# Kernel optimization log

Hardware: AMD Instinct MI355X
Metric: run time of the kernel (lower is better)

Reference implementation:

```python
import jax, jax.numpy as jnp
import numpy as np

B, S, D, H = 4, 2048, 768, 12
DH = D // H  # 64


def setup_inputs() -> dict:
    key = jax.random.key(0)
    ks = jax.random.split(key, 7)
    return {
        "sequences": jax.random.normal(ks[0], (B, S, D), dtype=jnp.float32),
        "wq": jax.random.normal(ks[1], (H, DH, DH), dtype=jnp.float32) / np.sqrt(DH),
        "bq": jax.random.normal(ks[2], (H, DH), dtype=jnp.float32) * 0.02,
        "wk": jax.random.normal(ks[3], (H, DH, DH), dtype=jnp.float32) / np.sqrt(DH),
        "bk": jax.random.normal(ks[4], (H, DH), dtype=jnp.float32) * 0.02,
        "wv": jax.random.normal(ks[5], (H, DH, DH), dtype=jnp.float32) / np.sqrt(DH),
        "bv": jax.random.normal(ks[6], (H, DH), dtype=jnp.float32) * 0.02,
    }


def reference(sequences, wq, bq, wk, bk, wv, bv):
    # split channels into heads: [B, S, H, DH]
    xh = sequences.reshape(B, S, H, DH)
    # per-head linear projections (weight applied as x @ W^T + b, matching nn.Linear)
    q = jnp.einsum("bshd,hed->bshe", xh, wq) + bq  # [B,S,H,DH]
    k = jnp.einsum("bshd,hed->bshe", xh, wk) + bk
    v = jnp.einsum("bshd,hed->bshe", xh, wv) + bv
    scale = 1.0 / np.sqrt(DH).astype(np.float32)
    scores = jnp.einsum("bqhd,bkhd->bhqk", q, k) * scale  # [B,H,S,S]
    attn = jax.nn.softmax(scores, axis=-1)
    out = jnp.einsum("bhqk,bkhd->bqhd", attn, v)  # [B,S,H,DH]
    return out.reshape(B, S, D)
```

## Files before the change

kernel.cpp:

```cpp
#include <hip/hip_runtime.h>

#define NB 4
#define NS 2048
#define ND 768
#define NH 12
#define NDH 64
#define NT (NS / 128)
#define XPITCH 72
#define SSCALE 0.18033688011112043f

typedef __bf16 bf16x8 __attribute__((ext_vector_type(8)));
typedef float  f32x4  __attribute__((ext_vector_type(4)));
typedef unsigned int u32;

#define MFMA16(a, b, c) __builtin_amdgcn_mfma_f32_16x16x32_bf16(a, b, c, 0, 0, 0)

__device__ __forceinline__ u32 packbf(float a, float b) {
    u32 ua = __builtin_bit_cast(u32, a) + 0x8000u;
    u32 ub = __builtin_bit_cast(u32, b) + 0x8000u;
    return __builtin_amdgcn_perm(ub, ua, 0x07060302u);
}

__device__ __forceinline__ bf16x8 cvt8(float4 a, float4 b) {
    union { u32 u[4]; bf16x8 v; } r;
    r.u[0] = packbf(a.x, a.y); r.u[1] = packbf(a.z, a.w);
    r.u[2] = packbf(b.x, b.y); r.u[3] = packbf(b.z, b.w);
    return r.v;
}

__device__ __forceinline__ __bf16 f2bf(float f) {
    u32 u = __builtin_bit_cast(u32, f) + 0x8000u;
    unsigned short s = (unsigned short)(u >> 16);
    return __builtin_bit_cast(__bf16, s);
}

__global__ __launch_bounds__(256, 4) void proj_kernel(
    const float* __restrict__ x,
    const float* __restrict__ wq, const float* __restrict__ bq,
    const float* __restrict__ wk, const float* __restrict__ bk,
    const float* __restrict__ wv, const float* __restrict__ bv,
    __bf16* __restrict__ qws, __bf16* __restrict__ kws, __bf16* __restrict__ vtws)
{
    const int st = blockIdx.x, h = blockIdx.y, b = blockIdx.z;
    const int s0 = st * 64;
    const int tid = threadIdx.x;

    __shared__ __align__(16) __bf16 Xs[64 * XPITCH];
    __shared__ __align__(16) __bf16 Tv[64 * XPITCH];

    const int r = tid >> 2, f = tid & 3;
    const int lane = tid & 63, w = tid >> 6, col = lane & 15, quad = lane >> 4;

    const size_t wrow = (size_t)(h * NDH + w * 16 + col) * NDH;
    const float* wq0 = wq + wrow + quad * 8;
    const float* wk0 = wk + wrow + quad * 8;
    const float* wv0 = wv + wrow + quad * 8;
    const bf16x8 wqa0 = cvt8(*(const float4*)(wq0),      *(const float4*)(wq0 + 4));
    const bf16x8 wqa1 = cvt8(*(const float4*)(wq0 + 32), *(const float4*)(wq0 + 36));
    const bf16x8 wka0 = cvt8(*(const float4*)(wk0),      *(const float4*)(wk0 + 4));
    const bf16x8 wka1 = cvt8(*(const float4*)(wk0 + 32), *(const float4*)(wk0 + 36));
    const bf16x8 wva0 = cvt8(*(const float4*)(wv0),      *(const float4*)(wv0 + 4));
    const bf16x8 wva1 = cvt8(*(const float4*)(wv0 + 32), *(const float4*)(wv0 + 36));

    float bqs[4], bks[4], bvs[4];
#pragma unroll
    for (int rr = 0; rr < 4; ++rr) {
        const int e = h * NDH + w * 16 + quad * 4 + rr;
        bqs[rr] = bq[e] * SSCALE;
        bks[rr] = bk[e];
        bvs[rr] = bv[e];
    }

    const size_t bh = (size_t)(b * NH + h);

    {
        const float* xrow = x + (size_t)(b * NS + s0 + r) * ND + h * NDH + f * 16;
        const float4 v0 = *(const float4*)(xrow);
        const float4 v1 = *(const float4*)(xrow + 4);
        const float4 v2 = *(const float4*)(xrow + 8);
        const float4 v3 = *(const float4*)(xrow + 12);
        *(bf16x8*)&Xs[r * XPITCH + f * 16]     = cvt8(v0, v1);
        *(bf16x8*)&Xs[r * XPITCH + f * 16 + 8] = cvt8(v2, v3);
    }
    __syncthreads();

#pragma unroll
    for (int nt = 0; nt < 4; ++nt) {
        const bf16x8 xb0 = *(const bf16x8*)&Xs[(nt * 16 + col) * XPITCH + quad * 8];
        const bf16x8 xb1 = *(const bf16x8*)&Xs[(nt * 16 + col) * XPITCH + 32 + quad * 8];
        f32x4 aq = {0.f, 0.f, 0.f, 0.f};
        f32x4 ak = {0.f, 0.f, 0.f, 0.f};
        f32x4 av = {0.f, 0.f, 0.f, 0.f};
        aq = MFMA16(wqa0, xb0, aq); aq = MFMA16(wqa1, xb1, aq);
        ak = MFMA16(wka0, xb0, ak); ak = MFMA16(wka1, xb1, ak);
        av = MFMA16(wva0, xb0, av); av = MFMA16(wva1, xb1, av);

        union { u32 u[2]; uint2 v; } pq, pk;
        pq.u[0] = packbf(fmaf(aq[0], SSCALE, bqs[0]), fmaf(aq[1], SSCALE, bqs[1]));
        pq.u[1] = packbf(fmaf(aq[2], SSCALE, bqs[2]), fmaf(aq[3], SSCALE, bqs[3]));
        pk.u[0] = packbf(ak[0] + bks[0], ak[1] + bks[1]);
        pk.u[1] = packbf(ak[2] + bks[2], ak[3] + bks[3]);
        const size_t goff = (bh * NS + s0 + nt * 16 + col) * NDH + w * 16 + quad * 4;
        *(uint2*)(qws + goff) = pq.v;
        *(uint2*)(kws + goff) = pk.v;

        const int pos = ((nt >> 1) << 5) + ((col >> 2) << 3) + ((nt & 1) << 2) + (col & 3);
#pragma unroll
        for (int rr = 0; rr < 4; ++rr)
            Tv[(w * 16 + quad * 4 + rr) * XPITCH + pos] = f2bf(av[rr] + bvs[rr]);
    }
    __syncthreads();

    {
        const uint4 v0 = *(const uint4*)&Tv[r * XPITCH + f * 16];
        const uint4 v1 = *(const uint4*)&Tv[r * XPITCH + f * 16 + 8];
        __bf16* vdst = vtws + (bh * NDH + r) * NS + s0 + f * 16;
        *(uint4*)vdst = v0; *(uint4*)(vdst + 8) = v1;
    }
}

__global__ __launch_bounds__(256, 3) void attn_kernel(
    const __bf16* __restrict__ qws, const __bf16* __restrict__ kws,
    const __bf16* __restrict__ vtws, float* __restrict__ out)
{
    const int bid = blockIdx.x;
    const int xcd = bid & 7;
    const int j   = bid >> 3;
    const int g   = xcd * 6 + (j >> 5);
    const int qt  = j & 31;
    const int h   = g % NH;
    const int b   = g / NH;

    const int q0 = qt * 64;
    const int tid = threadIdx.x;

    __shared__ __align__(16) unsigned char smem[36864];
    __bf16* lds = (__bf16*)smem;
    float* slabA = (float*)smem;
    float* slabB = (float*)(smem + 17408);
    float* lbuf  = (float*)(smem + 34816);

    const size_t bh = (size_t)(b * NH + h);
    const int lane = tid & 63, w = tid >> 6, col = lane & 15, quad = lane >> 4;
    const int L = lane;

    bf16x8 qb0[4], qb1[4];
#pragma unroll
    for (int nt = 0; nt < 4; ++nt) {
        const __bf16* qp = qws + (bh * NS + q0 + nt * 16 + col) * NDH + quad * 8;
        qb0[nt] = *(const bf16x8*)(qp);
        qb1[nt] = *(const bf16x8*)(qp + 32);
    }

    const __bf16* ksrc = kws + bh * (size_t)(NS * NDH)
                       + (size_t)(w * 32 + (L >> 3)) * NDH + ((L & 7) ^ (L >> 3)) * 8;
    const __bf16* vsrc = vtws + bh * (size_t)(NDH * NS)
                       + (size_t)(L >> 2) * NS + w * 32 + ((L & 3) ^ ((L >> 3) & 3)) * 8;
    const int kb_lds = w * 2048 + L * 8;
    const int vb_lds = 8192 + w * 2048 + L * 8;

    const int cx7 = col & 7;
    int ka_off[2][2], va_off[4];
#pragma unroll
    for (int mt = 0; mt < 2; ++mt) {
        const int base = w * 2048 + (mt * 16 + col) * 64;
        ka_off[mt][0] = base + ((quad)     ^ cx7) * 8;
        ka_off[mt][1] = base + ((quad + 4) ^ cx7) * 8;
    }
#pragma unroll
    for (int dt = 0; dt < 4; ++dt)
        va_off[dt] = 8192 + w * 2048 + (dt * 16 + col) * 32 + (quad ^ ((col >> 1) & 3)) * 8;

    float l[4] = {0.f, 0.f, 0.f, 0.f};
    f32x4 o[4][4];
#pragma unroll
    for (int dt = 0; dt < 4; ++dt)
#pragma unroll
        for (int nt = 0; nt < 4; ++nt) o[dt][nt] = (f32x4){0.f, 0.f, 0.f, 0.f};

    uint4 kstg[4], vstg[4];
#pragma unroll
    for (int i = 0; i < 4; ++i) kstg[i] = *(const uint4*)(ksrc + i * 512);
#pragma unroll
    for (int i = 0; i < 4; ++i) vstg[i] = *(const uint4*)(vsrc + (size_t)i * 16 * NS);
#pragma unroll
    for (int i = 0; i < 4; ++i) *(uint4*)&lds[kb_lds + i * 512] = kstg[i];
#pragma unroll
    for (int i = 0; i < 4; ++i) *(uint4*)&lds[vb_lds + i * 512] = vstg[i];

    for (int kt = 0; kt < NT; ++kt) {
        if (kt + 1 < NT) {
            const __bf16* ks = ksrc + (size_t)(kt + 1) * 8192;
            const __bf16* vs = vsrc + (kt + 1) * 128;
#pragma unroll
            for (int i = 0; i < 4; ++i) kstg[i] = *(const uint4*)(ks + i * 512);
#pragma unroll
            for (int i = 0; i < 4; ++i) vstg[i] = *(const uint4*)(vs + (size_t)i * 16 * NS);
        }

        bf16x8 ka[2][2], va[4];
#pragma unroll
        for (int mt = 0; mt < 2; ++mt) {
            ka[mt][0] = *(const bf16x8*)&lds[ka_off[mt][0]];
            ka[mt][1] = *(const bf16x8*)&lds[ka_off[mt][1]];
        }
#pragma unroll
        for (int dt = 0; dt < 4; ++dt) va[dt] = *(const bf16x8*)&lds[va_off[dt]];

        __builtin_amdgcn_s_setprio(1);
#pragma unroll
        for (int nt = 0; nt < 4; ++nt) {
            f32x4 sA = {0.f, 0.f, 0.f, 0.f};
            f32x4 sB = {0.f, 0.f, 0.f, 0.f};
            sA = MFMA16(ka[0][0], qb0[nt], sA); sA = MFMA16(ka[0][1], qb1[nt], sA);
            sB = MFMA16(ka[1][0], qb0[nt], sB); sB = MFMA16(ka[1][1], qb1[nt], sB);

            const float p0 = __builtin_amdgcn_exp2f(sA[0]);
            const float p1 = __builtin_amdgcn_exp2f(sA[1]);
            const float p2 = __builtin_amdgcn_exp2f(sA[2]);
            const float p3 = __builtin_amdgcn_exp2f(sA[3]);
            const float p4 = __builtin_amdgcn_exp2f(sB[0]);
            const float p5 = __builtin_amdgcn_exp2f(sB[1]);
            const float p6 = __builtin_amdgcn_exp2f(sB[2]);
            const float p7 = __builtin_amdgcn_exp2f(sB[3]);
            l[nt] += ((p0 + p1) + (p2 + p3)) + ((p4 + p5) + (p6 + p7));

            union { u32 u[4]; bf16x8 v; } pb;
            pb.u[0] = packbf(p0, p1);
            pb.u[1] = packbf(p2, p3);
            pb.u[2] = packbf(p4, p5);
            pb.u[3] = packbf(p6, p7);

#pragma unroll
            for (int dt = 0; dt < 4; ++dt)
                o[dt][nt] = MFMA16(va[dt], pb.v, o[dt][nt]);
        }
        __builtin_amdgcn_s_setprio(0);

        if (kt + 1 < NT) {
#pragma unroll
            for (int i = 0; i < 4; ++i) *(uint4*)&lds[kb_lds + i * 512] = kstg[i];
#pragma unroll
            for (int i = 0; i < 4; ++i) *(uint4*)&lds[vb_lds + i * 512] = vstg[i];
        }
    }

#pragma unroll
    for (int nt = 0; nt < 4; ++nt) {
        l[nt] += __shfl_xor(l[nt], 16, 64);
        l[nt] += __shfl_xor(l[nt], 32, 64);
    }

    __syncthreads();
    if (quad == 0) {
#pragma unroll
        for (int nt = 0; nt < 4; ++nt)
            lbuf[w * 64 + nt * 16 + col] = l[nt];
    }
    __syncthreads();

    float scale[4];
#pragma unroll
    for (int nt = 0; nt < 4; ++nt) {
        const int qi = nt * 16 + col;
        const float Lt = (lbuf[qi] + lbuf[64 + qi]) + (lbuf[128 + qi] + lbuf[192 + qi]);
        scale[nt] = 1.0f / Lt;
    }
    __syncthreads();
#pragma unroll
    for (int dt = 0; dt < 4; ++dt)
#pragma unroll
        for (int nt = 0; nt < 4; ++nt) o[dt][nt] *= scale[nt];

    if (w == 0 || w == 2) {
        float* s = (w == 0) ? slabA : slabB;
#pragma unroll
        for (int dt = 0; dt < 4; ++dt)
#pragma unroll
            for (int nt = 0; nt < 4; ++nt)
                *(f32x4*)&s[(nt * 16 + col) * 68 + dt * 16 + quad * 4] = o[dt][nt];
    }
    __syncthreads();
    if (w == 1 || w == 3) {
        float* s = (w == 1) ? slabA : slabB;
#pragma unroll
        for (int dt = 0; dt < 4; ++dt)
#pragma unroll
            for (int nt = 0; nt < 4; ++nt) {
                f32x4* p = (f32x4*)&s[(nt * 16 + col) * 68 + dt * 16 + quad * 4];
                *p = *p + o[dt][nt];
            }
    }
    __syncthreads();

    const int qr = tid >> 2, fq = tid & 3;
#pragma unroll
    for (int j2 = 0; j2 < 4; ++j2) {
        const f32x4 a = *(const f32x4*)&slabA[qr * 68 + fq * 16 + j2 * 4];
        const f32x4 c = *(const f32x4*)&slabB[qr * 68 + fq * 16 + j2 * 4];
        *(f32x4*)&out[(size_t)(b * NS + q0 + qr) * ND + h * NDH + fq * 16 + j2 * 4] = a + c;
    }
}

extern "C" void kernel_launch(void* const* d_in, const int* in_sizes, int n_in,
                              void* d_out, int out_size, void* d_ws, size_t ws_size,
                              hipStream_t stream) {
    (void)in_sizes; (void)n_in; (void)out_size; (void)ws_size;
    const float* x  = (const float*)d_in[0];
    const float* wq = (const float*)d_in[1];
    const float* bq = (const float*)d_in[2];
    const float* wk = (const float*)d_in[3];
    const float* bk = (const float*)d_in[4];
    const float* wv = (const float*)d_in[5];
    const float* bv = (const float*)d_in[6];
    float* out = (float*)d_out;

    __bf16* qws  = (__bf16*)d_ws;
    __bf16* kws  = qws + (size_t)NB * NH * NS * NDH;
    __bf16* vtws = kws + (size_t)NB * NH * NS * NDH;

    dim3 grid(NS / 64, NH, NB);
    proj_kernel<<<grid, 256, 0, stream>>>(x, wq, bq, wk, bk, wv, bv, qws, kws, vtws);
    attn_kernel<<<dim3(NS / 64 * NH * NB), 256, 0, stream>>>(qws, kws, vtws, out);
}
```

Baseline: 180.8 us.

## Write Q/K/V in MFMA-fragment order and load attention operands directly from global

The projection kernel now writes Q, K and transposed V into a pre-swizzled layout that matches each lane's MFMA operand fragment. The attention kernel drops the LDS staging of K/V and its register-staged copies. It instead loads fragments straight from global memory with coalesced 16-byte reads, double-buffered in registers across two key tiles. This removes LDS writes, reads and bank-conflict swizzling, and the setprio hints are dropped. The trade-off is more direct global/L2 traffic per wave and added register pressure.

```diff
diff --git a/kernel.cpp b/kernel.cpp
--- a/kernel.cpp
+++ b/kernel.cpp
@@ -33,6 +33,7 @@
     unsigned short s = (unsigned short)(u >> 16);
     return __builtin_bit_cast(__bf16, s);
 }
+
 
 __global__ __launch_bounds__(256, 4) void proj_kernel(
     const float* __restrict__ x,
@@ -84,6 +85,13 @@
     }
     __syncthreads();
 
+    const int e0 = w * 16 + quad * 4;
+    const int jj = e0 >> 5;
+    const int qa = (e0 >> 3) & 3;
+    const int hf = (e0 >> 2) & 1;
+    const int Lf = qa * 16 + col;
+    const int kt = st >> 1;
+
 #pragma unroll
     for (int nt = 0; nt < 4; ++nt) {
         const bf16x8 xb0 = *(const bf16x8*)&Xs[(nt * 16 + col) * XPITCH + quad * 8];
@@ -100,9 +108,13 @@
         pq.u[1] = packbf(fmaf(aq[2], SSCALE, bqs[2]), fmaf(aq[3], SSCALE, bqs[3]));
         pk.u[0] = packbf(ak[0] + bks[0], ak[1] + bks[1]);
         pk.u[1] = packbf(ak[2] + bks[2], ak[3] + bks[3]);
-        const size_t goff = (bh * NS + s0 + nt * 16 + col) * NDH + w * 16 + quad * 4;
-        *(uint2*)(qws + goff) = pq.v;
-        *(uint2*)(kws + goff) = pk.v;
+
+        const int wa = (st & 1) * 2 + (nt >> 1);
+        const int mt = nt & 1;
+        const size_t kidx = ((((((size_t)bh * 16 + kt) * 4 + wa) * 2 + mt) * 2 + jj) * 64 + Lf) * 8 + hf * 4;
+        const size_t qidx = (((((size_t)bh * 32 + st) * 4 + nt) * 2 + jj) * 64 + Lf) * 8 + hf * 4;
+        *(uint2*)(kws + kidx) = pk.v;
+        *(uint2*)(qws + qidx) = pq.v;
 
         const int pos = ((nt >> 1) << 5) + ((col >> 2) << 3) + ((nt & 1) << 2) + (col & 3);
 #pragma unroll
@@ -114,8 +126,14 @@
     {
         const uint4 v0 = *(const uint4*)&Tv[r * XPITCH + f * 16];
         const uint4 v1 = *(const uint4*)&Tv[r * XPITCH + f * 16 + 8];
-        __bf16* vdst = vtws + (bh * NDH + r) * NS + s0 + f * 16;
-        *(uint4*)vdst = v0; *(uint4*)(vdst + 8) = v1;
+        const int wv_ = (st & 1) * 2 + (f >> 1);
+        const int dtv = r >> 4;
+        const int colv = r & 15;
+        const int L0 = ((f & 1) * 2 + 0) * 16 + colv;
+        const int L1 = ((f & 1) * 2 + 1) * 16 + colv;
+        const size_t vbase = (((size_t)bh * 16 + kt) * 4 + wv_) * 4 + dtv;
+        *(uint4*)(vtws + (vbase * 64 + L0) * 8) = v0;
+        *(uint4*)(vtws + (vbase * 64 + L1) * 8) = v1;
     }
 }
 
@@ -134,42 +152,26 @@
     const int q0 = qt * 64;
     const int tid = threadIdx.x;
 
-    __shared__ __align__(16) unsigned char smem[36864];
-    __bf16* lds = (__bf16*)smem;
+    __shared__ __align__(16) unsigned char smem[35840];
     float* slabA = (float*)smem;
     float* slabB = (float*)(smem + 17408);
     float* lbuf  = (float*)(smem + 34816);
 
     const size_t bh = (size_t)(b * NH + h);
     const int lane = tid & 63, w = tid >> 6, col = lane & 15, quad = lane >> 4;
-    const int L = lane;
 
     bf16x8 qb0[4], qb1[4];
-#pragma unroll
-    for (int nt = 0; nt < 4; ++nt) {
-        const __bf16* qp = qws + (bh * NS + q0 + nt * 16 + col) * NDH + quad * 8;
-        qb0[nt] = *(const bf16x8*)(qp);
-        qb1[nt] = *(const bf16x8*)(qp + 32);
-    }
-
-    const __bf16* ksrc = kws + bh * (size_t)(NS * NDH)
-                       + (size_t)(w * 32 + (L >> 3)) * NDH + ((L & 7) ^ (L >> 3)) * 8;
-    const __bf16* vsrc = vtws + bh * (size_t)(NDH * NS)
-                       + (size_t)(L >> 2) * NS + w * 32 + ((L & 3) ^ ((L >> 3) & 3)) * 8;
-    const int kb_lds = w * 2048 + L * 8;
-    const int vb_lds = 8192 + w * 2048 + L * 8;
-
-    const int cx7 = col & 7;
-    int ka_off[2][2], va_off[4];
-#pragma unroll
-    for (int mt = 0; mt < 2; ++mt) {
-        const int base = w * 2048 + (mt * 16 + col) * 64;
-        ka_off[mt][0] = base + ((quad)     ^ cx7) * 8;
-        ka_off[mt][1] = base + ((quad + 4) ^ cx7) * 8;
-    }
-#pragma unroll
-    for (int dt = 0; dt < 4; ++dt)
-        va_off[dt] = 8192 + w * 2048 + (dt * 16 + col) * 32 + (quad ^ ((col >> 1) & 3)) * 8;
+    {
+        const __bf16* qp = qws + (size_t)bh * 131072 + (size_t)qt * 4096 + lane * 8;
+#pragma unroll
+        for (int nt = 0; nt < 4; ++nt) {
+            qb0[nt] = *(const bf16x8*)(qp + nt * 1024);
+            qb1[nt] = *(const bf16x8*)(qp + nt * 1024 + 512);
+        }
+    }
+
+    const __bf16* kb = kws  + (size_t)bh * 131072 + w * 2048 + lane * 8;
+    const __bf16* vb = vtws + (size_t)bh * 131072 + w * 2048 + lane * 8;
 
     float l[4] = {0.f, 0.f, 0.f, 0.f};
     f32x4 o[4][4];
@@ -178,36 +180,18 @@
 #pragma unroll
         for (int nt = 0; nt < 4; ++nt) o[dt][nt] = (f32x4){0.f, 0.f, 0.f, 0.f};
 
-    uint4 kstg[4], vstg[4];
-#pragma unroll
-    for (int i = 0; i < 4; ++i) kstg[i] = *(const uint4*)(ksrc + i * 512);
-#pragma unroll
-    for (int i = 0; i < 4; ++i) vstg[i] = *(const uint4*)(vsrc + (size_t)i * 16 * NS);
-#pragma unroll
-    for (int i = 0; i < 4; ++i) *(uint4*)&lds[kb_lds + i * 512] = kstg[i];
-#pragma unroll
-    for (int i = 0; i < 4; ++i) *(uint4*)&lds[vb_lds + i * 512] = vstg[i];
-
-    for (int kt = 0; kt < NT; ++kt) {
-        if (kt + 1 < NT) {
-            const __bf16* ks = ksrc + (size_t)(kt + 1) * 8192;
-            const __bf16* vs = vsrc + (kt + 1) * 128;
-#pragma unroll
-            for (int i = 0; i < 4; ++i) kstg[i] = *(const uint4*)(ks + i * 512);
-#pragma unroll
-            for (int i = 0; i < 4; ++i) vstg[i] = *(const uint4*)(vs + (size_t)i * 16 * NS);
-        }
-
-        bf16x8 ka[2][2], va[4];
-#pragma unroll
-        for (int mt = 0; mt < 2; ++mt) {
-            ka[mt][0] = *(const bf16x8*)&lds[ka_off[mt][0]];
-            ka[mt][1] = *(const bf16x8*)&lds[ka_off[mt][1]];
-        }
-#pragma unroll
-        for (int dt = 0; dt < 4; ++dt) va[dt] = *(const bf16x8*)&lds[va_off[dt]];
-
-        __builtin_amdgcn_s_setprio(1);
+#define LOADK(dst, kt) do { \
+        const __bf16* _p = kb + (size_t)(kt) * 8192; \
+        dst[0][0] = *(const bf16x8*)(_p);        dst[0][1] = *(const bf16x8*)(_p + 512); \
+        dst[1][0] = *(const bf16x8*)(_p + 1024); dst[1][1] = *(const bf16x8*)(_p + 1536); \
+    } while (0)
+#define LOADV(dst, kt) do { \
+        const __bf16* _p = vb + (size_t)(kt) * 8192; \
+        dst[0] = *(const bf16x8*)(_p);        dst[1] = *(const bf16x8*)(_p + 512); \
+        dst[2] = *(const bf16x8*)(_p + 1024); dst[3] = *(const bf16x8*)(_p + 1536); \
+    } while (0)
+
+    auto compute = [&](const bf16x8 (&ka)[2][2], const bf16x8 (&va)[4]) {
 #pragma unroll
         for (int nt = 0; nt < 4; ++nt) {
             f32x4 sA = {0.f, 0.f, 0.f, 0.f};
@@ -235,15 +219,18 @@
             for (int dt = 0; dt < 4; ++dt)
                 o[dt][nt] = MFMA16(va[dt], pb.v, o[dt][nt]);
         }
-        __builtin_amdgcn_s_setprio(0);
-
-        if (kt + 1 < NT) {
-#pragma unroll
-            for (int i = 0; i < 4; ++i) *(uint4*)&lds[kb_lds + i * 512] = kstg[i];
-#pragma unroll
-            for (int i = 0; i < 4; ++i) *(uint4*)&lds[vb_lds + i * 512] = vstg[i];
-        }
-    }
+    };
+
+    bf16x8 kc[2][2], vc[4], kn[2][2], vn[4];
+    LOADK(kc, 0); LOADV(vc, 0);
+    for (int kt2 = 0; kt2 < NT; kt2 += 2) {
+        LOADK(kn, kt2 + 1); LOADV(vn, kt2 + 1);
+        compute(kc, vc);
+        if (kt2 + 2 < NT) { LOADK(kc, kt2 + 2); LOADV(vc, kt2 + 2); }
+        compute(kn, vn);
+    }
+#undef LOADK
+#undef LOADV
 
 #pragma unroll
     for (int nt = 0; nt < 4; ++nt) {
```

Result: slower. 285.0 us (+57.6%).
